# Kernel optimization log

Measured on AMD Instinct MI355X. Metric: run time of the kernel, lower is better.

## Reference

```python
import jax, jax.numpy as jnp
import numpy as np

B, S, HID, NH, HD, E, K = 8, 1024, 1024, 16, 64, 8, 2
IDIM = 2 * HD  # expert internal dim
EPS = 1e-5


def layer_norm(x, g, b):
    m = jnp.mean(x, axis=-1, keepdims=True)
    v = jnp.mean(jnp.square(x - m), axis=-1, keepdims=True)
    return (x - m) * jax.lax.rsqrt(v + EPS) * g + b


def setup_inputs() -> dict:
    key = jax.random.key(0)
    ks = jax.random.split(key, 12)
    n = jax.random.normal
    return {
        "queries": n(ks[0], (B, S, HID), jnp.float32),
        "keys": n(ks[1], (B, S, HID), jnp.float32),
        "values": n(ks[2], (B, S, HID), jnp.float32),
        "memorys": n(ks[3], (B, NH, S, HD), jnp.float32),
        "Wq": n(ks[4], (HD, HD), jnp.float32) * 0.02,
        "Wk": n(ks[5], (HD, HD), jnp.float32) * 0.02,
        "Wv": n(ks[6], (HD, HD), jnp.float32) * 0.02,
        "forget_gate": n(ks[7], (HD,), jnp.float32),
        "gate_W": n(ks[8], (E, HD), jnp.float32) * 0.02,
        "gate_b": jnp.zeros((E,), jnp.float32),
        "ln1_g": jnp.ones((E, HD), jnp.float32),
        "ln1_b": jnp.zeros((E, HD), jnp.float32),
        "W1": n(ks[9], (E, IDIM, HD), jnp.float32) * 0.02,
        "ln2_g": jnp.ones((E, IDIM), jnp.float32),
        "ln2_b": jnp.zeros((E, IDIM), jnp.float32),
        "W2": n(ks[10], (E, HD, IDIM), jnp.float32) * 0.02,
        "b2": jnp.zeros((E, HD), jnp.float32),
    }


def reference(queries, keys, values, memorys, Wq, Wk, Wv, forget_gate,
              gate_W, gate_b, ln1_g, ln1_b, W1, ln2_g, ln2_b, W2, b2):
    bsz, seq, _ = queries.shape
    gelu = lambda x: jax.nn.gelu(x, approximate=False)

    # head split: [B,S,HID] -> [B,NH,S,HD]
    q = queries.reshape(bsz, seq, NH, HD).transpose(0, 2, 1, 3)
    k = keys.reshape(bsz, seq, NH, HD).transpose(0, 2, 1, 3)
    v = values.reshape(bsz, seq, NH, HD).transpose(0, 2, 1, 3)

    q_ = q @ Wq.T
    k_ = k @ Wk.T
    v_ = v @ Wv.T

    # gated memory cell
    cell = k_ * v_ + forget_gate * memorys
    current_memorys = (1.0 - forget_gate) * cell + forget_gate * memorys
    cell_values = q_ * current_memorys  # [B,NH,S,HD]

    # token-mixing MoE (per-token, over last dim)
    x = cell_values.reshape(-1, HD)  # [N, HD], N = B*NH*S
    logits = x @ gate_W.T + gate_b  # [N, E]
    topv, topi = jax.lax.top_k(logits, K)  # [N, K]
    # sparse combine weights [N, E] (raw gate values, as in the original)
    w = jnp.sum(jax.nn.one_hot(topi, E, dtype=x.dtype) * topv[..., None], axis=1)

    def expert_fwd(g1, b1, w1, g2, b2_, w2, bias2):
        h = gelu(layer_norm(x, g1, b1)) @ w1.T      # [N, IDIM]
        h = gelu(layer_norm(h, g2, b2_)) @ w2.T + bias2  # [N, HD]
        return h

    all_out = jax.vmap(expert_fwd)(ln1_g, ln1_b, W1, ln2_g, ln2_b, W2, b2)  # [E,N,HD]
    moe = jnp.einsum('ne,end->nd', w, all_out)  # [N, HD]

    token_mixing = moe.reshape(bsz, NH, seq, HD).transpose(0, 2, 1, 3).reshape(bsz, seq, NH * HD)
    return token_mixing, current_memorys
```

## Files before the change

### kernel.cpp

```cpp
#include <hip/hip_runtime.h>
#include <stdint.h>

typedef unsigned short u16;
typedef unsigned int   u32;
typedef unsigned long long u64;
typedef __attribute__((ext_vector_type(8))) short short8;
typedef __attribute__((ext_vector_type(4))) short s16x4;
typedef __attribute__((ext_vector_type(4))) float f32x4;

#define B_    8
#define S_    1024
#define HID_  1024
#define NH_   16
#define HD_   64
#define E_    8
#define IDIM_ 128
#define NTOK  (B_*NH_*S_)

#define CSTRIDE 16
#define XROW 65

__device__ __forceinline__ float bf2f(u16 u){ return __uint_as_float(((u32)u) << 16); }
__device__ __forceinline__ u16 f2bf(float f){
    u32 u = __float_as_uint(f);
    u32 r = u + 0x7fffu + ((u >> 16) & 1u);
    return (u16)(r >> 16);
}
__device__ __forceinline__ short8 frag8(const float* __restrict__ p){
    float4 a = *(const float4*)p;
    float4 b = *(const float4*)(p + 4);
    short8 r;
    r[0]=(short)f2bf(a.x); r[1]=(short)f2bf(a.y); r[2]=(short)f2bf(a.z); r[3]=(short)f2bf(a.w);
    r[4]=(short)f2bf(b.x); r[5]=(short)f2bf(b.y); r[6]=(short)f2bf(b.z); r[7]=(short)f2bf(b.w);
    return r;
}
__device__ __forceinline__ float gelu_exact(float x){
    return 0.5f * x * (1.0f + erff(x * 0.70710678118654752f));
}
__device__ __forceinline__ float gelu_f(float x){
    float z = 1.5957691216057308f * (x + 0.044715f * x * x * x);
    float e = __expf(z);
    float t = 1.0f - 2.0f / (e + 1.0f);
    return 0.5f * x * (1.0f + t);
}

__global__ void k_zero(u32* c){
    c[threadIdx.x] = 0;
}

__global__ __launch_bounds__(256,2) void k_proj(
    const float* __restrict__ qin, const float* __restrict__ kin, const float* __restrict__ vin,
    const float* __restrict__ mem,
    const float* __restrict__ Wq, const float* __restrict__ Wk, const float* __restrict__ Wv,
    const float* __restrict__ fg,
    const float* __restrict__ gW, const float* __restrict__ gB,
    const float* __restrict__ l1g, const float* __restrict__ l1b,
    float* __restrict__ cur_out, float* __restrict__ out0,
    uint4* __restrict__ topiv, u32* __restrict__ pcount, int writeXg)
{
    __shared__ float sT[4][64*XROW];
    __shared__ float sGW[512], sGB[8];
    __shared__ float sG1[8*XROW], sB1g[8*XROW];
    __shared__ u32 sWc1[4][8], sWc2[4][8];

    const int tid  = threadIdx.x;
    const int lane = tid & 63;
    const int wid  = tid >> 6;
    const int m    = lane & 15;
    const int kg   = lane >> 4;

    for (int i = tid; i < 512; i += 256){
        sGW[i] = gW[i];
        const int e = i >> 6, d = i & 63;
        sG1[e*XROW+d] = l1g[i]; sB1g[e*XROW+d] = l1b[i];
    }
    if (tid < 8) sGB[tid] = gB[tid];

    const int slab  = blockIdx.x;
    const int chunk = slab & 3, h = (slab >> 2) & 15, b = slab >> 6;
    const int tw    = chunk*256 + wid*64;

    float* sW = &sT[wid][0];

    const float* kbase = kin + ((size_t)b*S_)*HID_ + h*64;
    const float* vbase = vin + ((size_t)b*S_)*HID_ + h*64;
    const float* qbase = qin + ((size_t)b*S_)*HID_ + h*64;

    f32x4 accK[4][4], accV[4][4];
    const f32x4 z = {0.f,0.f,0.f,0.f};
    #pragma unroll
    for (int i=0;i<4;i++){ accK[i][0]=z;accK[i][1]=z;accK[i][2]=z;accK[i][3]=z;
                           accV[i][0]=z;accV[i][1]=z;accV[i][2]=z;accV[i][3]=z; }

    #pragma unroll
    for (int kk=0; kk<2; kk++){
        const int k0 = kk*32 + kg*8;
        short8 aF[4], bF[4];
        #pragma unroll
        for (int mt=0; mt<4; mt++) aF[mt] = frag8(kbase + (size_t)(tw + mt*16 + m)*HID_ + k0);
        #pragma unroll
        for (int ct=0; ct<4; ct++) bF[ct] = frag8(Wk + (ct*16 + m)*64 + k0);
        #pragma unroll
        for (int mt=0; mt<4; mt++)
            #pragma unroll
            for (int ct=0; ct<4; ct++)
                accK[mt][ct] = __builtin_amdgcn_mfma_f32_16x16x32_bf16(aF[mt], bF[ct], accK[mt][ct], 0,0,0);
    }
    #pragma unroll
    for (int kk=0; kk<2; kk++){
        const int k0 = kk*32 + kg*8;
        short8 aF[4], bF[4];
        #pragma unroll
        for (int mt=0; mt<4; mt++) aF[mt] = frag8(vbase + (size_t)(tw + mt*16 + m)*HID_ + k0);
        #pragma unroll
        for (int ct=0; ct<4; ct++) bF[ct] = frag8(Wv + (ct*16 + m)*64 + k0);
        #pragma unroll
        for (int mt=0; mt<4; mt++)
            #pragma unroll
            for (int ct=0; ct<4; ct++)
                accV[mt][ct] = __builtin_amdgcn_mfma_f32_16x16x32_bf16(aF[mt], bF[ct], accV[mt][ct], 0,0,0);
    }

    const size_t nb = ((size_t)(b*NH_ + h)) << 10;
    float fgv[4];
    #pragma unroll
    for (int ct=0; ct<4; ct++) fgv[ct] = fg[ct*16 + m];

    #pragma unroll
    for (int mt=0; mt<4; mt++){
        #pragma unroll
        for (int r=0; r<4; r++){
            const int tok = tw + mt*16 + kg*4 + r;
            const size_t rowo = (nb + (size_t)tok)*64;
            #pragma unroll
            for (int ct=0; ct<4; ct++){
                const int d = ct*16 + m;
                const float kd = accK[mt][ct][r];
                const float vd = accV[mt][ct][r];
                const float f  = fgv[ct];
                const float mv = mem[rowo + d];
                const float cell = kd*vd + f*mv;
                const float cur  = (1.0f - f)*cell + f*mv;
                accK[mt][ct][r] = cur;
                cur_out[rowo + d] = cur;
            }
        }
    }

    f32x4 accQ[4][4];
    #pragma unroll
    for (int i=0;i<4;i++){ accQ[i][0]=z;accQ[i][1]=z;accQ[i][2]=z;accQ[i][3]=z; }

    #pragma unroll
    for (int kk=0; kk<2; kk++){
        const int k0 = kk*32 + kg*8;
        short8 aF[4], bF[4];
        #pragma unroll
        for (int mt=0; mt<4; mt++) aF[mt] = frag8(qbase + (size_t)(tw + mt*16 + m)*HID_ + k0);
        #pragma unroll
        for (int ct=0; ct<4; ct++) bF[ct] = frag8(Wq + (ct*16 + m)*64 + k0);
        #pragma unroll
        for (int mt=0; mt<4; mt++)
            #pragma unroll
            for (int ct=0; ct<4; ct++)
                accQ[mt][ct] = __builtin_amdgcn_mfma_f32_16x16x32_bf16(aF[mt], bF[ct], accQ[mt][ct], 0,0,0);
    }

    if (!writeXg){
        #pragma unroll
        for (int mt=0; mt<4; mt++){
            #pragma unroll
            for (int r=0; r<4; r++){
                const int tok = tw + mt*16 + kg*4 + r;
                const size_t po = ((size_t)(b*S_ + tok)*NH_ + h)*64;
                #pragma unroll
                for (int ct=0; ct<4; ct++){
                    const int d = ct*16 + m;
                    out0[po + d] = accQ[mt][ct][r] * accK[mt][ct][r];
                }
            }
        }
        return;
    }

    __syncthreads();

    #pragma unroll
    for (int mt=0; mt<4; mt++){
        #pragma unroll
        for (int r=0; r<4; r++){
            const int trow = mt*16 + kg*4 + r;
            #pragma unroll
            for (int ct=0; ct<4; ct++){
                const int d = ct*16 + m;
                sW[trow*XROW + d] = accQ[mt][ct][r] * accK[mt][ct][r];
            }
        }
    }

    const int tok = tw + lane;
    const int n   = (int)(nb + tok);
    float rx[64];
    {
        const float* xr = &sW[lane*XROW];
        #pragma unroll
        for (int d = 0; d < 64; d++) rx[d] = xr[d];
    }

    float lg[8];
    #pragma unroll
    for (int e = 0; e < 8; e++) lg[e] = sGB[e];
    float s0 = 0.f, s1 = 0.f;
    #pragma unroll
    for (int d = 0; d < 64; d++){
        const float xv = rx[d];
        s0 += xv; s1 += xv*xv;
        #pragma unroll
        for (int e = 0; e < 8; e++) lg[e] += sGW[e*64 + d] * xv;
    }

    int i1 = 0; float v1 = lg[0];
    #pragma unroll
    for (int e = 1; e < 8; e++){ if (lg[e] > v1){ v1 = lg[e]; i1 = e; } }
    int i2 = -1; float v2 = -3.0e38f;
    #pragma unroll
    for (int e = 0; e < 8; e++){ if (e != i1 && lg[e] > v2){ v2 = lg[e]; i2 = e; } }

    topiv[n] = make_uint4((u32)i1, (u32)i2, __float_as_uint(v1), __float_as_uint(v2));

    #pragma unroll
    for (int e = 0; e < 8; e++){
        u64 m1 = __ballot(i1 == e);
        u64 m2 = __ballot(i2 == e);
        if (lane == 0){ sWc1[wid][e] = (u32)__popcll(m1); sWc2[wid][e] = (u32)__popcll(m2); }
    }

    {
        const float mu = s0 * (1.0f/64.0f);
        const float rs = rsqrtf(s1 * (1.0f/64.0f) - mu*mu + 1e-5f);
        u32* xw = (u32*)&sW[lane*XROW];
        #pragma unroll
        for (int half = 0; half < 2; half++){
            const int ee = half ? i2 : i1;
            const float* g1 = &sG1[ee*XROW];
            const float* b1 = &sB1g[ee*XROW];
            #pragma unroll
            for (int dp = 0; dp < 32; dp++){
                const float v0 = gelu_f((rx[2*dp+0] - mu)*rs*g1[2*dp+0] + b1[2*dp+0]);
                const float vb = gelu_f((rx[2*dp+1] - mu)*rs*g1[2*dp+1] + b1[2*dp+1]);
                xw[half*32 + dp] = (u32)f2bf(v0) | ((u32)f2bf(vb) << 16);
            }
        }
    }

    {
        u16* xgbase = (u16*)out0 + ((nb + (size_t)tw) << 7);
        #pragma unroll
        for (int j = 0; j < 16; j++){
            const int idx = j*64 + lane;
            const int row = idx >> 4, dc = idx & 15;
            const u32* p = (const u32*)&sW[row*XROW] + dc*4;
            uint4 v; v.x = p[0]; v.y = p[1]; v.z = p[2]; v.w = p[3];
            ((uint4*)xgbase)[idx] = v;
        }
    }

    __syncthreads();
    if (tid < 8){
        u32 t = sWc1[0][tid] + sWc1[1][tid] + sWc1[2][tid] + sWc1[3][tid]
              + sWc2[0][tid] + sWc2[1][tid] + sWc2[2][tid] + sWc2[3][tid];
        pcount[blockIdx.x*8 + tid] = t;
    }
}

__global__ __launch_bounds__(256,2) void k_gate(
    float* __restrict__ x_io, const float* __restrict__ gW, const float* __restrict__ gB,
    const float* __restrict__ l1g, const float* __restrict__ l1b,
    uint4* __restrict__ topiv, u32* __restrict__ counts, int writeXg)
{
    __shared__ float sX[256*XROW];
    __shared__ float sGW[512], sGB[8];
    __shared__ float sG1[8*XROW], sB1g[8*XROW];
    __shared__ u32 sWc[4][8];

    const int tid = threadIdx.x;
    for (int i = tid; i < 512; i += 256){
        sGW[i] = gW[i];
        const int e = i >> 6, d = i & 63;
        sG1[e*XROW+d] = l1g[i]; sB1g[e*XROW+d] = l1b[i];
    }
    if (tid < 8) sGB[tid] = gB[tid];

    const int rowBase = blockIdx.x * 256;
    const float* gsrc = x_io + ((size_t)rowBase << 6);
    #pragma unroll
    for (int j = 0; j < 16; j++){
        const int idx = j*256 + tid;
        const int row = idx >> 4, dc = idx & 15;
        float4 v = ((const float4*)gsrc)[idx];
        float* p = &sX[row*XROW + dc*4];
        p[0]=v.x; p[1]=v.y; p[2]=v.z; p[3]=v.w;
    }
    __syncthreads();

    const int pos = rowBase + tid;
    const int h  = pos & (NH_-1);
    const int bs = pos >> 4;
    const int s  = bs & (S_-1), b = bs >> 10;
    const int n  = ((b*NH_ + h) << 10) + s;

    float rx[64];
    {
        const float* xr = &sX[tid*XROW];
        #pragma unroll
        for (int d = 0; d < 64; d++) rx[d] = xr[d];
    }

    float lg[8];
    #pragma unroll
    for (int e = 0; e < 8; e++) lg[e] = sGB[e];
    float s0 = 0.f, s1 = 0.f;
    #pragma unroll
    for (int d = 0; d < 64; d++){
        const float xv = rx[d];
        s0 += xv; s1 += xv*xv;
        #pragma unroll
        for (int e = 0; e < 8; e++) lg[e] += sGW[e*64 + d] * xv;
    }

    int i1 = 0; float v1 = lg[0];
    #pragma unroll
    for (int e = 1; e < 8; e++){ if (lg[e] > v1){ v1 = lg[e]; i1 = e; } }
    int i2 = -1; float v2 = -3.0e38f;
    #pragma unroll
    for (int e = 0; e < 8; e++){ if (e != i1 && lg[e] > v2){ v2 = lg[e]; i2 = e; } }

    topiv[n] = make_uint4((u32)i1, (u32)i2, __float_as_uint(v1), __float_as_uint(v2));

    {
        const int lane = tid & 63;
        const int w    = tid >> 6;
        #pragma unroll
        for (int e = 0; e < 8; e++){
            u64 m1 = __ballot(i1 == e);
            u64 m2 = __ballot(i2 == e);
            if (lane == 0) sWc[w][e] = (u32)(__popcll(m1) + __popcll(m2));
        }
    }
    __syncthreads();

    if (tid < 8){
        u32 t = sWc[0][tid] + sWc[1][tid] + sWc[2][tid] + sWc[3][tid];
        if (t) atomicAdd(&counts[tid*CSTRIDE], t);
    }
    (void)writeXg;
}

__global__ __launch_bounds__(256,2) void k_scatter(
    const uint4* __restrict__ topiv, u32* __restrict__ counts, u32* __restrict__ cursors,
    const u32* __restrict__ pc,
    const float* __restrict__ W1, const float* __restrict__ W2,
    u16* __restrict__ wB1, u16* __restrict__ wB2,
    u32* __restrict__ bucket, int2* __restrict__ slots, int useMfma)
{
    __shared__ u32 sC1[4][8], sC2[4][8];
    __shared__ u32 sB1[4][8], sB2w[4][8];
    __shared__ u32 pcL[4096];
    __shared__ u32 sTot[8], sBase[8];

    const int tid = threadIdx.x;
    const int j   = blockIdx.x;
    const int n   = j*256 + tid;

    if (useMfma){
        if (n < 65536) wB1[n] = f2bf(W1[n]);
        else           wB2[n - 65536] = f2bf(W2[n - 65536]);
        for (int i = tid; i < 4096; i += 256) pcL[i] = pc[i];
    }

    uint4 t = topiv[n];
    const int i1 = (int)t.x, i2 = (int)t.y;

    const int lane = tid & 63;
    const int w    = tid >> 6;
    const u64 low = (1ull << lane) - 1ull;

    u64 myM1 = 0, myM2 = 0;
    #pragma unroll
    for (int e = 0; e < 8; e++){
        u64 m1 = __ballot(i1 == e);
        u64 m2 = __ballot(i2 == e);
        if (i1 == e) myM1 = m1;
        if (i2 == e) myM2 = m2;
        if (lane == 0){ sC1[w][e] = (u32)__popcll(m1); sC2[w][e] = (u32)__popcll(m2); }
    }
    __syncthreads();

    if (useMfma){
        if (tid < 8){
            const int e = tid;
            u32 tot = 0, base = 0;
            for (int i = 0; i < 512; i++){
                const u32 c = pcL[i*8 + e];
                tot += c;
                if (i < j) base += c;
            }
            sTot[e] = tot; sBase[e] = base;
            if (j == 0) counts[e*CSTRIDE] = tot;
        }
        __syncthreads();
        if (tid < 8){
            const int e = tid;
            u32 off = 0;
            #pragma unroll
            for (int ee = 0; ee < 8; ee++){ if (ee < e) off += sTot[ee]; }
            u32 run = off + sBase[e];
            #pragma unroll
            for (int ww = 0; ww < 4; ww++){
                sB1[ww][e] = run; run += sC1[ww][e];
                sB2w[ww][e] = run; run += sC2[ww][e];
            }
        }
        __syncthreads();
    } else {
        int off[8]; int acc = 0;
        #pragma unroll
        for (int e = 0; e < 8; e++){ off[e] = acc; acc += (int)counts[e*CSTRIDE]; }
        if (tid < 8){
            const int e = tid;
            u32 tot = 0;
            #pragma unroll
            for (int ww = 0; ww < 4; ww++) tot += sC1[ww][e] + sC2[ww][e];
            u32 base = tot ? atomicAdd(&cursors[e*CSTRIDE], tot) : 0;
            u32 run = (u32)off[e] + base;
            #pragma unroll
            for (int ww = 0; ww < 4; ww++){
                sB1[ww][e] = run; run += sC1[ww][e];
                sB2w[ww][e] = run; run += sC2[ww][e];
            }
        }
        __syncthreads();
    }

    const int slot1 = (int)sB1[w][i1] + (int)__popcll(myM1 & low);
    const int slot2 = (int)sB2w[w][i2] + (int)__popcll(myM2 & low);

    bucket[slot1] = ((u32)n << 1);
    bucket[slot2] = ((u32)n << 1) | 1u;
    slots[n] = make_int2(slot1, slot2);
}

__global__ __launch_bounds__(256,4) void k_expert_mfma(
    const float* __restrict__ x_src, const u32* __restrict__ bucket, const u32* __restrict__ counts,
    const u16* __restrict__ wB1, const u16* __restrict__ wB2,
    const float* __restrict__ l2g, const float* __restrict__ l2b,
    const float* __restrict__ b2,  u16* __restrict__ aout)
{
    const int e = blockIdx.x >> 10;
    const int c = blockIdx.x & 1023;
    const int cnt = (int)counts[e*CSTRIDE];
    const int aBase = c * 128;
    if (aBase >= cnt) return;

    int off = 0;
    #pragma unroll
    for (int ee = 0; ee < 8; ee++){ if (ee < e) off += (int)counts[ee*CSTRIDE]; }

    __shared__ __align__(16) u16 sH[4][32*128];
    __shared__ float sL2g[128], sL2b[128], sB2[64];

    const int tid = threadIdx.x;
    if (tid < 128){ sL2g[tid] = l2g[e*128+tid]; sL2b[tid] = l2b[e*128+tid]; }
    else if (tid < 192){ sB2[tid-128] = b2[e*64 + tid-128]; }
    __syncthreads();

    const int lane = tid & 63;
    const int w    = tid >> 6;
    const int m    = lane & 15;
    const int kg   = lane >> 4;
    const int tb   = aBase + w*32;
    char* sHw = (char*)(&sH[w][0]);

    const u16* xg = (const u16*)x_src;
    short8 aF[2][2];
    #pragma unroll
    for (int t = 0; t < 2; t++){
        int a = tb + t*16 + m; if (a > cnt-1) a = cnt-1;
        const u32 bv = bucket[off + a];
        const u16* rp = xg + (((size_t)(bv >> 1)) << 7) + (bv & 1u)*64;
        aF[t][0] = *(const short8*)(rp + kg*8);
        aF[t][1] = *(const short8*)(rp + 32 + kg*8);
    }

    const f32x4 z = {0.f,0.f,0.f,0.f};
    f32x4 acc1[2][8];
    #pragma unroll
    for (int t = 0; t < 2; t++)
        #pragma unroll
        for (int ct = 0; ct < 8; ct++) acc1[t][ct] = z;

    const u16* wB1e = wB1 + e*8192;
    #pragma unroll
    for (int kk = 0; kk < 2; kk++){
        const int k0 = kk*32 + kg*8;
        short8 bF[8];
        #pragma unroll
        for (int ct = 0; ct < 8; ct++)
            bF[ct] = *(const short8*)(wB1e + (ct*16 + m)*64 + k0);
        #pragma unroll
        for (int t = 0; t < 2; t++)
            #pragma unroll
            for (int ct = 0; ct < 8; ct++)
                acc1[t][ct] = __builtin_amdgcn_mfma_f32_16x16x32_bf16(aF[t][kk], bF[ct], acc1[t][ct], 0,0,0);
    }

    #pragma unroll
    for (int t = 0; t < 2; t++){
        #pragma unroll
        for (int r = 0; r < 4; r++){
            float p0 = 0.f, p1 = 0.f;
            #pragma unroll
            for (int ct = 0; ct < 8; ct++){ float v = acc1[t][ct][r]; p0 += v; p1 += v*v; }
            #pragma unroll
            for (int msk = 1; msk < 16; msk <<= 1){
                p0 += __shfl_xor(p0, msk);
                p1 += __shfl_xor(p1, msk);
            }
            const float mu = p0 * (1.0f/128.0f);
            const float rs = rsqrtf(p1 * (1.0f/128.0f) - mu*mu + 1e-5f);
            const int row = t*16 + kg*4 + r;
            #pragma unroll
            for (int ct = 0; ct < 8; ct++){
                const int col = ct*16 + m;
                *(u16*)(sHw + (((row<<8) + (col<<1)) ^ ((row&7)<<4)))
                    = f2bf(gelu_f((acc1[t][ct][r] - mu)*rs*sL2g[col] + sL2b[col]));
            }
        }
    }

    f32x4 acc2[2][4];
    #pragma unroll
    for (int t = 0; t < 2; t++)
        #pragma unroll
        for (int ct = 0; ct < 4; ct++) acc2[t][ct] = z;

    const u16* wB2e = wB2 + e*8192;
    #pragma unroll
    for (int kk = 0; kk < 4; kk++){
        const int k0 = kk*32 + kg*8;
        short8 aF2[2], bF2[4];
        #pragma unroll
        for (int t = 0; t < 2; t++){
            const int row = t*16 + m;
            aF2[t] = *(const short8*)(sHw + (((row<<8) + (k0<<1)) ^ ((row&7)<<4)));
        }
        #pragma unroll
        for (int ct = 0; ct < 4; ct++)
            bF2[ct] = *(const short8*)(wB2e + (ct*16 + m)*128 + k0);
        #pragma unroll
        for (int t = 0; t < 2; t++)
            #pragma unroll
            for (int ct = 0; ct < 4; ct++)
                acc2[t][ct] = __builtin_amdgcn_mfma_f32_16x16x32_bf16(aF2[t], bF2[ct], acc2[t][ct], 0,0,0);
    }

    #pragma unroll
    for (int t = 0; t < 2; t++){
        #pragma unroll
        for (int r = 0; r < 4; r++){
            const int row = t*16 + kg*4 + r;
            #pragma unroll
            for (int ct = 0; ct < 4; ct++){
                const int col = ct*16 + m;
                *(u16*)(sHw + (((row<<7) + (col<<1)) ^ ((row&7)<<4)))
                    = f2bf(acc2[t][ct][r] + sB2[col]);
            }
        }
    }

    #pragma unroll
    for (int it = 0; it < 4; it++){
        const int idx = it*64 + lane;
        const int row = idx >> 3, qq = idx & 7;
        if (tb + row < cnt){
            uint4 v = *(const uint4*)(sHw + (((row<<7) + (qq<<4)) ^ ((row&7)<<4)));
            *(uint4*)(aout + ((size_t)(off + tb + row) << 6) + qq*8) = v;
        }
    }
}

__global__ __launch_bounds__(256,2) void k_expert(
    const float* __restrict__ x_src, const u32* __restrict__ bucket, const u32* __restrict__ counts,
    const float* __restrict__ W1,  const float* __restrict__ W2,
    const float* __restrict__ l1g, const float* __restrict__ l1b,
    const float* __restrict__ l2g, const float* __restrict__ l2b,
    const float* __restrict__ b2,  u16* __restrict__ aout)
{
    const int e = blockIdx.x >> 9;
    const int c = blockIdx.x & 511;
    const int cnt = (int)counts[e*CSTRIDE];
    const int aBase = c * 256;
    if (aBase >= cnt) return;

    int off = 0;
    for (int ee = 0; ee < 8; ee++){ if (ee < e) off += (int)counts[ee*CSTRIDE]; }

    __shared__ float sW1[8192];
    __shared__ float sW2T[128*68];
    __shared__ float sL1g[64], sL1b[64], sL2g[128], sL2b[128], sB2[64];
    const int tid = threadIdx.x;
    for (int i = tid; i < 8192; i += 256){
        sW1[i] = W1[e*8192 + i];
        int d = i >> 7, j = i & 127;
        sW2T[j*68 + d] = W2[e*8192 + i];
    }
    if (tid < 64){ sL1g[tid] = l1g[e*64+tid]; sL1b[tid] = l1b[e*64+tid]; sB2[tid] = b2[e*64+tid]; }
    if (tid < 128){ sL2g[tid] = l2g[e*128+tid]; sL2b[tid] = l2b[e*128+tid]; }
    __syncthreads();

    const int a = aBase + tid;
    if (a >= cnt) return;
    const u32 nv = bucket[off + a] >> 1;
    const int s = (int)(nv & (S_-1));
    const int h = (int)((nv >> 10) & (NH_-1));
    const int b = (int)(nv >> 14);
    const u32 pos32 = (u32)((b*S_ + s)*NH_ + h);

    float g[64];
    #pragma unroll
    for (int i = 0; i < 16; i++){
        float4 t = ((const float4*)(x_src + (size_t)pos32*64))[i];
        g[i*4+0]=t.x; g[i*4+1]=t.y; g[i*4+2]=t.z; g[i*4+3]=t.w;
    }

    float s0 = 0.f, s1 = 0.f;
    #pragma unroll
    for (int d = 0; d < 64; d++){ s0 += g[d]; s1 += g[d]*g[d]; }
    float m  = s0 * (1.0f/64.0f);
    float va = s1 * (1.0f/64.0f) - m*m;
    float rs = rsqrtf(va + 1e-5f);
    #pragma unroll
    for (int d = 0; d < 64; d++) g[d] = gelu_exact((g[d]-m)*rs*sL1g[d] + sL1b[d]);

    u32 hpk[64];
    float hs = 0.f, hs2 = 0.f;
    for (int jp = 0; jp < 64; jp++){
        float h0, h1;
        {
            float a0=0.f,a1=0.f,a2=0.f,a3=0.f;
            const float4* w4 = (const float4*)&sW1[(2*jp)*64];
            #pragma unroll
            for (int i = 0; i < 16; i++){
                float4 ww = w4[i];
                a0 += ww.x*g[i*4+0]; a1 += ww.y*g[i*4+1]; a2 += ww.z*g[i*4+2]; a3 += ww.w*g[i*4+3];
            }
            h0 = (a0+a1)+(a2+a3);
        }
        {
            float a0=0.f,a1=0.f,a2=0.f,a3=0.f;
            const float4* w4 = (const float4*)&sW1[(2*jp+1)*64];
            #pragma unroll
            for (int i = 0; i < 16; i++){
                float4 ww = w4[i];
                a0 += ww.x*g[i*4+0]; a1 += ww.y*g[i*4+1]; a2 += ww.z*g[i*4+2]; a3 += ww.w*g[i*4+3];
            }
            h1 = (a0+a1)+(a2+a3);
        }
        hs += h0 + h1; hs2 += h0*h0 + h1*h1;
        hpk[jp] = (u32)f2bf(h0) | ((u32)f2bf(h1) << 16);
    }
    float m2  = hs  * (1.0f/128.0f);
    float va2 = hs2 * (1.0f/128.0f) - m2*m2;
    float rs2 = rsqrtf(va2 + 1e-5f);

    float acc[64];
    #pragma unroll
    for (int d = 0; d < 64; d++) acc[d] = sB2[d];
    for (int j = 0; j < 128; j++){
        float hj = bf2f((u16)((j & 1) ? (hpk[j>>1] >> 16) : (hpk[j>>1] & 0xffffu)));
        float gh = gelu_exact((hj - m2)*rs2*sL2g[j] + sL2b[j]);
        const float4* w2t = (const float4*)&sW2T[j*68];
        #pragma unroll
        for (int d4 = 0; d4 < 16; d4++){
            float4 w = w2t[d4];
            acc[d4*4+0] += gh * w.x;
            acc[d4*4+1] += gh * w.y;
            acc[d4*4+2] += gh * w.z;
            acc[d4*4+3] += gh * w.w;
        }
    }

    u16* op = aout + (size_t)(off + a) * 64;
    #pragma unroll
    for (int dc = 0; dc < 8; dc++){
        uint4 o;
        o.x = (u32)f2bf(acc[dc*8+0]) | ((u32)f2bf(acc[dc*8+1]) << 16);
        o.y = (u32)f2bf(acc[dc*8+2]) | ((u32)f2bf(acc[dc*8+3]) << 16);
        o.z = (u32)f2bf(acc[dc*8+4]) | ((u32)f2bf(acc[dc*8+5]) << 16);
        o.w = (u32)f2bf(acc[dc*8+6]) | ((u32)f2bf(acc[dc*8+7]) << 16);
        ((uint4*)op)[dc] = o;
    }
}

__global__ __launch_bounds__(256,4) void k_combine(
    const u16* __restrict__ aout, const uint4* __restrict__ topiv,
    const int2* __restrict__ slots, float* __restrict__ out0)
{
    const int tid = threadIdx.x;
    const int p   = blockIdx.x*16 + (tid >> 4);
    const int cq  = tid & 15;

    const int h  = p & (NH_-1);
    const int bs = p >> 4;
    const int b  = bs >> 10, s = bs & (S_-1);
    const int n  = ((b*NH_ + h) << 10) + s;

    uint4 t = topiv[n];
    float w1 = __uint_as_float(t.z), w2 = __uint_as_float(t.w);
    int2 sl = slots[n];

    uint2 ua = *(const uint2*)(aout + (size_t)sl.x*64 + cq*4);
    uint2 ub = *(const uint2*)(aout + (size_t)sl.y*64 + cq*4);

    float4 o;
    o.x = w1*bf2f((u16)(ua.x & 0xffffu)) + w2*bf2f((u16)(ub.x & 0xffffu));
    o.y = w1*bf2f((u16)(ua.x >> 16))     + w2*bf2f((u16)(ub.x >> 16));
    o.z = w1*bf2f((u16)(ua.y & 0xffffu)) + w2*bf2f((u16)(ub.y & 0xffffu));
    o.w = w1*bf2f((u16)(ua.y >> 16))     + w2*bf2f((u16)(ub.y >> 16));
    *(float4*)(out0 + (size_t)p*64 + cq*4) = o;
}

extern "C" void kernel_launch(void* const* d_in, const int* in_sizes, int n_in,
                              void* d_out, int out_size, void* d_ws, size_t ws_size,
                              hipStream_t stream)
{
    const float* qin = (const float*)d_in[0];
    const float* kin = (const float*)d_in[1];
    const float* vin = (const float*)d_in[2];
    const float* mem = (const float*)d_in[3];
    const float* Wq  = (const float*)d_in[4];
    const float* Wk  = (const float*)d_in[5];
    const float* Wv  = (const float*)d_in[6];
    const float* fg  = (const float*)d_in[7];
    const float* gW  = (const float*)d_in[8];
    const float* gB  = (const float*)d_in[9];
    const float* l1g = (const float*)d_in[10];
    const float* l1b = (const float*)d_in[11];
    const float* W1  = (const float*)d_in[12];
    const float* l2g = (const float*)d_in[13];
    const float* l2b = (const float*)d_in[14];
    const float* W2  = (const float*)d_in[15];
    const float* b2  = (const float*)d_in[16];

    float* out0 = (float*)d_out;
    float* out1 = out0 + (size_t)NTOK * 64;

    char* ws = (char*)d_ws;
    u16*   aout   = (u16*)(ws);
    u32*   pc     = (u32*)(ws);
    uint4* topiv  = (uint4*)(ws + (size_t)33554432);
    int2*  slots  = (int2*)(ws + (size_t)35651584);
    u32*   bucket = (u32*)(ws + (size_t)36700160);
    u32*   counts = (u32*)(ws + (size_t)37748736);
    u32*   cursors = (u32*)(ws + (size_t)37749248);
    u16*   wB1    = (u16*)(ws + (size_t)37749760);
    u16*   wB2    = (u16*)(ws + (size_t)37880832);
    const size_t WS_NEED = 38011904;

    (void)in_sizes; (void)n_in; (void)out_size;

    const bool use_mfma = (ws_size >= WS_NEED);

    if (use_mfma){
        k_proj   <<<512, 256, 0, stream>>>(qin, kin, vin, mem, Wq, Wk, Wv, fg,
                                           gW, gB, l1g, l1b, out1, out0,
                                           topiv, pc, 1);
        k_scatter<<<512, 256, 0, stream>>>(topiv, counts, cursors, pc,
                                           W1, W2, wB1, wB2, bucket, slots, 1);
        k_expert_mfma<<<E_*1024, 256, 0, stream>>>(out0, bucket, counts, wB1, wB2,
                                                   l2g, l2b, b2, aout);
        k_combine<<<NTOK/16, 256, 0, stream>>>(aout, topiv, slots, out0);
    } else {
        k_zero   <<<1, 256, 0, stream>>>(counts);
        k_proj   <<<512, 256, 0, stream>>>(qin, kin, vin, mem, Wq, Wk, Wv, fg,
                                           gW, gB, l1g, l1b, out1, out0,
                                           topiv, pc, 0);
        k_gate   <<<NTOK/256, 256, 0, stream>>>(out0, gW, gB, l1g, l1b, topiv, counts, 0);
        k_scatter<<<NTOK/256, 256, 0, stream>>>(topiv, counts, cursors, pc,
                                                W1, W2, wB1, wB2, bucket, slots, 0);
        k_expert <<<E_*512, 256, 0, stream>>>(out0, bucket, counts, W1, W2,
                                              l1g, l1b, l2g, l2b, b2, aout);
        k_combine<<<NTOK/16, 256, 0, stream>>>(aout, topiv, slots, out0);
    }
}
```

Before: 300.4 us.

## Split gate/LN epilogue into two 32-token phases with half-row per lane

The per-wave transpose buffer shrinks from 64 to 32 rows. The gate/LN/GELU epilogue now runs in two phases, with each pair of lanes sharing one token: each lane handles half of the 64 features and the partial sums and logits are combined with shuffles. This cuts shared-memory usage and per-thread register arrays (rx goes from 64 to 32 floats), which should raise occupancy and spread the per-token work across all lanes. The cost is extra shuffles, duplicated top-k computation in both lanes of each pair, and ballot masking to avoid double counting.

```diff
diff --git a/kernel.cpp b/kernel.cpp
--- a/kernel.cpp
+++ b/kernel.cpp
@@ -58,7 +58,7 @@
     float* __restrict__ cur_out, float* __restrict__ out0,
     uint4* __restrict__ topiv, u32* __restrict__ pcount, int writeXg)
 {
-    __shared__ float sT[4][64*XROW];
+    __shared__ float sT[4][32*XROW];
     __shared__ float sGW[512], sGB[8];
     __shared__ float sG1[8*XROW], sB1g[8*XROW];
     __shared__ u32 sWc1[4][8], sWc2[4][8];
@@ -185,84 +185,107 @@
 
     __syncthreads();
 
-    #pragma unroll
-    for (int mt=0; mt<4; mt++){
-        #pragma unroll
-        for (int r=0; r<4; r++){
-            const int trow = mt*16 + kg*4 + r;
-            #pragma unroll
-            for (int ct=0; ct<4; ct++){
-                const int d = ct*16 + m;
-                sW[trow*XROW + d] = accQ[mt][ct][r] * accK[mt][ct][r];
-            }
-        }
-    }
-
-    const int tok = tw + lane;
-    const int n   = (int)(nb + tok);
-    float rx[64];
-    {
-        const float* xr = &sW[lane*XROW];
-        #pragma unroll
-        for (int d = 0; d < 64; d++) rx[d] = xr[d];
-    }
-
-    float lg[8];
-    #pragma unroll
-    for (int e = 0; e < 8; e++) lg[e] = sGB[e];
-    float s0 = 0.f, s1 = 0.f;
-    #pragma unroll
-    for (int d = 0; d < 64; d++){
-        const float xv = rx[d];
-        s0 += xv; s1 += xv*xv;
-        #pragma unroll
-        for (int e = 0; e < 8; e++) lg[e] += sGW[e*64 + d] * xv;
-    }
-
-    int i1 = 0; float v1 = lg[0];
-    #pragma unroll
-    for (int e = 1; e < 8; e++){ if (lg[e] > v1){ v1 = lg[e]; i1 = e; } }
-    int i2 = -1; float v2 = -3.0e38f;
-    #pragma unroll
-    for (int e = 0; e < 8; e++){ if (e != i1 && lg[e] > v2){ v2 = lg[e]; i2 = e; } }
-
-    topiv[n] = make_uint4((u32)i1, (u32)i2, __float_as_uint(v1), __float_as_uint(v2));
-
-    #pragma unroll
-    for (int e = 0; e < 8; e++){
-        u64 m1 = __ballot(i1 == e);
-        u64 m2 = __ballot(i2 == e);
-        if (lane == 0){ sWc1[wid][e] = (u32)__popcll(m1); sWc2[wid][e] = (u32)__popcll(m2); }
-    }
-
-    {
-        const float mu = s0 * (1.0f/64.0f);
-        const float rs = rsqrtf(s1 * (1.0f/64.0f) - mu*mu + 1e-5f);
-        u32* xw = (u32*)&sW[lane*XROW];
-        #pragma unroll
-        for (int half = 0; half < 2; half++){
-            const int ee = half ? i2 : i1;
-            const float* g1 = &sG1[ee*XROW];
-            const float* b1 = &sB1g[ee*XROW];
-            #pragma unroll
-            for (int dp = 0; dp < 32; dp++){
-                const float v0 = gelu_f((rx[2*dp+0] - mu)*rs*g1[2*dp+0] + b1[2*dp+0]);
-                const float vb = gelu_f((rx[2*dp+1] - mu)*rs*g1[2*dp+1] + b1[2*dp+1]);
-                xw[half*32 + dp] = (u32)f2bf(v0) | ((u32)f2bf(vb) << 16);
-            }
-        }
-    }
-
-    {
-        u16* xgbase = (u16*)out0 + ((nb + (size_t)tw) << 7);
-        #pragma unroll
-        for (int j = 0; j < 16; j++){
-            const int idx = j*64 + lane;
-            const int row = idx >> 4, dc = idx & 15;
-            const u32* p = (const u32*)&sW[row*XROW] + dc*4;
-            uint4 v; v.x = p[0]; v.y = p[1]; v.z = p[2]; v.w = p[3];
-            ((uint4*)xgbase)[idx] = v;
-        }
+    const u64 evenMask = 0x5555555555555555ull;
+    u32 c1a[8] = {0,0,0,0,0,0,0,0};
+    u32 c2a[8] = {0,0,0,0,0,0,0,0};
+
+    #pragma unroll
+    for (int ph = 0; ph < 2; ph++){
+        #pragma unroll
+        for (int mt2=0; mt2<2; mt2++){
+            const int mt = ph*2 + mt2;
+            #pragma unroll
+            for (int r=0; r<4; r++){
+                const int trow = mt2*16 + kg*4 + r;
+                #pragma unroll
+                for (int ct=0; ct<4; ct++){
+                    const int d = ct*16 + m;
+                    sW[trow*XROW + d] = accQ[mt][ct][r] * accK[mt][ct][r];
+                }
+            }
+        }
+
+        const int trow = lane >> 1;
+        const int hf   = lane & 1;
+        const int tok  = tw + ph*32 + trow;
+        const int n    = (int)(nb + tok);
+
+        float rx[32];
+        {
+            const float* xr = &sW[trow*XROW + hf*32];
+            #pragma unroll
+            for (int d = 0; d < 32; d++) rx[d] = xr[d];
+        }
+
+        float lg[8];
+        #pragma unroll
+        for (int e = 0; e < 8; e++) lg[e] = 0.f;
+        float s0 = 0.f, s1 = 0.f;
+        #pragma unroll
+        for (int d = 0; d < 32; d++){
+            const float xv = rx[d];
+            s0 += xv; s1 += xv*xv;
+            #pragma unroll
+            for (int e = 0; e < 8; e++) lg[e] += sGW[e*64 + hf*32 + d] * xv;
+        }
+        s0 += __shfl_xor(s0, 1);
+        s1 += __shfl_xor(s1, 1);
+        #pragma unroll
+        for (int e = 0; e < 8; e++) lg[e] += __shfl_xor(lg[e], 1);
+        #pragma unroll
+        for (int e = 0; e < 8; e++) lg[e] += sGB[e];
+
+        int i1 = 0; float v1 = lg[0];
+        #pragma unroll
+        for (int e = 1; e < 8; e++){ if (lg[e] > v1){ v1 = lg[e]; i1 = e; } }
+        int i2 = -1; float v2 = -3.0e38f;
+        #pragma unroll
+        for (int e = 0; e < 8; e++){ if (e != i1 && lg[e] > v2){ v2 = lg[e]; i2 = e; } }
+
+        if (hf == 0)
+            topiv[n] = make_uint4((u32)i1, (u32)i2, __float_as_uint(v1), __float_as_uint(v2));
+
+        #pragma unroll
+        for (int e = 0; e < 8; e++){
+            u64 m1 = __ballot(i1 == e) & evenMask;
+            u64 m2 = __ballot(i2 == e) & evenMask;
+            if (lane == 0){ c1a[e] += (u32)__popcll(m1); c2a[e] += (u32)__popcll(m2); }
+        }
+
+        {
+            const float mu = s0 * (1.0f/64.0f);
+            const float rs = rsqrtf(s1 * (1.0f/64.0f) - mu*mu + 1e-5f);
+            u32* xw = (u32*)&sW[trow*XROW];
+            #pragma unroll
+            for (int half = 0; half < 2; half++){
+                const int ee = half ? i2 : i1;
+                const float* g1 = &sG1[ee*XROW + hf*32];
+                const float* b1 = &sB1g[ee*XROW + hf*32];
+                #pragma unroll
+                for (int dp = 0; dp < 16; dp++){
+                    const float v0 = gelu_f((rx[2*dp+0] - mu)*rs*g1[2*dp+0] + b1[2*dp+0]);
+                    const float vb = gelu_f((rx[2*dp+1] - mu)*rs*g1[2*dp+1] + b1[2*dp+1]);
+                    xw[half*32 + hf*16 + dp] = (u32)f2bf(v0) | ((u32)f2bf(vb) << 16);
+                }
+            }
+        }
+
+        {
+            u16* xgbase = (u16*)out0 + ((nb + (size_t)(tw + ph*32)) << 7);
+            #pragma unroll
+            for (int j = 0; j < 8; j++){
+                const int idx = j*64 + lane;
+                const int row = idx >> 4, dc = idx & 15;
+                const u32* p = (const u32*)&sW[row*XROW] + dc*4;
+                uint4 v; v.x = p[0]; v.y = p[1]; v.z = p[2]; v.w = p[3];
+                ((uint4*)xgbase)[idx] = v;
+            }
+        }
+    }
+
+    if (lane == 0){
+        #pragma unroll
+        for (int e = 0; e < 8; e++){ sWc1[wid][e] = c1a[e]; sWc2[wid][e] = c2a[e]; }
     }
 
     __syncthreads();
```

After: 310.9 us. 1.03x slower.

## Fuse MoE combine into expert kernel via weighted atomic adds to output

Applied to the files above, without the earlier changes.

The expert MFMA kernel now scales each expert output row by its gate weight and atomically adds it straight into the final token-mixing layout. This removes the separate combine kernel, the bf16 intermediate expert-output buffer and the slots array. The gated activations move to a workspace buffer, and out0 is zeroed inside the scatter kernel so the atomics can accumulate into it. The trade is about 16.7M scattered fp32 global atomics plus an extra zero-fill pass over the output, in place of one streaming combine pass.

```diff
diff --git a/kernel.cpp b/kernel.cpp
--- a/kernel.cpp
+++ b/kernel.cpp
@@ -55,7 +55,7 @@
     const float* __restrict__ fg,
     const float* __restrict__ gW, const float* __restrict__ gB,
     const float* __restrict__ l1g, const float* __restrict__ l1b,
-    float* __restrict__ cur_out, float* __restrict__ out0,
+    float* __restrict__ cur_out, float* __restrict__ out0, u16* __restrict__ xg,
     uint4* __restrict__ topiv, u32* __restrict__ pcount, int writeXg)
 {
     __shared__ float sT[4][64*XROW];
@@ -254,7 +254,7 @@
     }
 
     {
-        u16* xgbase = (u16*)out0 + ((nb + (size_t)tw) << 7);
+        u16* xgbase = xg + ((nb + (size_t)tw) << 7);
         #pragma unroll
         for (int j = 0; j < 16; j++){
             const int idx = j*64 + lane;
@@ -361,7 +361,8 @@
     const u32* __restrict__ pc,
     const float* __restrict__ W1, const float* __restrict__ W2,
     u16* __restrict__ wB1, u16* __restrict__ wB2,
-    u32* __restrict__ bucket, int2* __restrict__ slots, int useMfma)
+    u32* __restrict__ bucket, int2* __restrict__ slots, float* __restrict__ out0z,
+    int useMfma)
 {
     __shared__ u32 sC1[4][8], sC2[4][8];
     __shared__ u32 sB1[4][8], sB2w[4][8];
@@ -376,6 +377,10 @@
         if (n < 65536) wB1[n] = f2bf(W1[n]);
         else           wB2[n - 65536] = f2bf(W2[n - 65536]);
         for (int i = tid; i < 4096; i += 256) pcL[i] = pc[i];
+        float4* zp = (float4*)out0z + (size_t)j*4096;
+        const float4 z4 = {0.f,0.f,0.f,0.f};
+        #pragma unroll
+        for (int k = 0; k < 16; k++) zp[k*256 + tid] = z4;
     }
 
     uint4 t = topiv[n];
@@ -447,14 +452,15 @@
 
     bucket[slot1] = ((u32)n << 1);
     bucket[slot2] = ((u32)n << 1) | 1u;
-    slots[n] = make_int2(slot1, slot2);
+    if (!useMfma) slots[n] = make_int2(slot1, slot2);
 }
 
 __global__ __launch_bounds__(256,4) void k_expert_mfma(
-    const float* __restrict__ x_src, const u32* __restrict__ bucket, const u32* __restrict__ counts,
+    const u16* __restrict__ xg, const u32* __restrict__ bucket, const u32* __restrict__ counts,
+    const uint4* __restrict__ topiv,
     const u16* __restrict__ wB1, const u16* __restrict__ wB2,
     const float* __restrict__ l2g, const float* __restrict__ l2b,
-    const float* __restrict__ b2,  u16* __restrict__ aout)
+    const float* __restrict__ b2,  float* __restrict__ out0)
 {
     const int e = blockIdx.x >> 10;
     const int c = blockIdx.x & 1023;
@@ -481,7 +487,6 @@
     const int tb   = aBase + w*32;
     char* sHw = (char*)(&sH[w][0]);
 
-    const u16* xg = (const u16*)x_src;
     short8 aF[2][2];
     #pragma unroll
     for (int t = 0; t < 2; t++){
@@ -569,22 +574,22 @@
         #pragma unroll
         for (int r = 0; r < 4; r++){
             const int row = t*16 + kg*4 + r;
-            #pragma unroll
-            for (int ct = 0; ct < 4; ct++){
-                const int col = ct*16 + m;
-                *(u16*)(sHw + (((row<<7) + (col<<1)) ^ ((row&7)<<4)))
-                    = f2bf(acc2[t][ct][r] + sB2[col]);
-            }
-        }
-    }
-
-    #pragma unroll
-    for (int it = 0; it < 4; it++){
-        const int idx = it*64 + lane;
-        const int row = idx >> 3, qq = idx & 7;
-        if (tb + row < cnt){
-            uint4 v = *(const uint4*)(sHw + (((row<<7) + (qq<<4)) ^ ((row&7)<<4)));
-            *(uint4*)(aout + ((size_t)(off + tb + row) << 6) + qq*8) = v;
+            const int gr  = tb + row;
+            if (gr < cnt){
+                const u32 bv = bucket[off + gr];
+                const u32 nn = bv >> 1;
+                const uint4 tv = topiv[nn];
+                const float wgt = __uint_as_float((bv & 1u) ? tv.w : tv.z);
+                const int ss = (int)(nn & (S_-1));
+                const int hh = (int)((nn >> 10) & (NH_-1));
+                const int bb = (int)(nn >> 14);
+                float* op = out0 + ((size_t)((bb*S_ + ss)*NH_ + hh) << 6);
+                #pragma unroll
+                for (int ct = 0; ct < 4; ct++){
+                    const int col = ct*16 + m;
+                    atomicAdd(&op[col], wgt*(acc2[t][ct][r] + sB2[col]));
+                }
+            }
         }
     }
 }
@@ -757,9 +762,10 @@
 
     char* ws = (char*)d_ws;
     u16*   aout   = (u16*)(ws);
-    u32*   pc     = (u32*)(ws);
+    u16*   xgbuf  = (u16*)(ws);
     uint4* topiv  = (uint4*)(ws + (size_t)33554432);
     int2*  slots  = (int2*)(ws + (size_t)35651584);
+    u32*   pc     = (u32*)(ws + (size_t)35651584);
     u32*   bucket = (u32*)(ws + (size_t)36700160);
     u32*   counts = (u32*)(ws + (size_t)37748736);
     u32*   cursors = (u32*)(ws + (size_t)37749248);
@@ -773,21 +779,20 @@
 
     if (use_mfma){
         k_proj   <<<512, 256, 0, stream>>>(qin, kin, vin, mem, Wq, Wk, Wv, fg,
-                                           gW, gB, l1g, l1b, out1, out0,
+                                           gW, gB, l1g, l1b, out1, out0, xgbuf,
                                            topiv, pc, 1);
         k_scatter<<<512, 256, 0, stream>>>(topiv, counts, cursors, pc,
-                                           W1, W2, wB1, wB2, bucket, slots, 1);
-        k_expert_mfma<<<E_*1024, 256, 0, stream>>>(out0, bucket, counts, wB1, wB2,
-                                                   l2g, l2b, b2, aout);
-        k_combine<<<NTOK/16, 256, 0, stream>>>(aout, topiv, slots, out0);
+                                           W1, W2, wB1, wB2, bucket, slots, out0, 1);
+        k_expert_mfma<<<E_*1024, 256, 0, stream>>>(xgbuf, bucket, counts, topiv,
+                                                   wB1, wB2, l2g, l2b, b2, out0);
     } else {
         k_zero   <<<1, 256, 0, stream>>>(counts);
         k_proj   <<<512, 256, 0, stream>>>(qin, kin, vin, mem, Wq, Wk, Wv, fg,
-                                           gW, gB, l1g, l1b, out1, out0,
+                                           gW, gB, l1g, l1b, out1, out0, xgbuf,
                                            topiv, pc, 0);
         k_gate   <<<NTOK/256, 256, 0, stream>>>(out0, gW, gB, l1g, l1b, topiv, counts, 0);
         k_scatter<<<NTOK/256, 256, 0, stream>>>(topiv, counts, cursors, pc,
-                                                W1, W2, wB1, wB2, bucket, slots, 0);
+                                                W1, W2, wB1, wB2, bucket, slots, out0, 0);
         k_expert <<<E_*512, 256, 0, stream>>>(out0, bucket, counts, W1, W2,
                                               l1g, l1b, l2g, l2b, b2, aout);
         k_combine<<<NTOK/16, 256, 0, stream>>>(aout, topiv, slots, out0);
```

Measured after the change: 316.1 us. 1.05x slower.
